# Performance work log

Hardware: AMD Instinct MI355X
Metric: run time of the kernel (lower is better)

The kernel has to match this reference:

```python
import jax, jax.numpy as jnp
import numpy as np

TOP_K = 2


def setup_inputs() -> dict:
    key = jax.random.key(0)
    ks = jax.random.split(key, 5)
    B, S, D, F, E = 4, 2048, 1024, 2048, 8
    sd = 1.0 / np.sqrt(D)
    sf = 1.0 / np.sqrt(F)
    return {
        "hidden_states": jax.random.normal(ks[0], (B, S, D), jnp.float32),
        "router_w1": jax.random.normal(ks[1], (D, 128), jnp.float32) * sd,
        "router_w2": jax.random.normal(ks[2], (128, E), jnp.float32) * (1.0 / np.sqrt(128)),
        "W1": jax.random.normal(ks[3], (E, D, F), jnp.float32) * sd,
        "W2": jax.random.normal(ks[4], (E, F, D), jnp.float32) * sf,
    }


def reference(hidden_states, router_w1, router_w2, W1, W2):
    B, S, D = hidden_states.shape
    E = W1.shape[0]
    # --- Router: MLP -> softmax -> top-k -> renormalize ---
    router_logits = jax.nn.silu(hidden_states @ router_w1) @ router_w2  # (B,S,E)
    router_probs = jax.nn.softmax(router_logits, axis=-1)
    top_vals, top_idx = jax.lax.top_k(router_probs, TOP_K)  # (B,S,K)
    routing_weights = top_vals / jnp.sum(top_vals, axis=-1, keepdims=True)

    # --- Dispatch/combine as dense combine-weight matrix (faithful to
    # weighted scatter-add combine in _grouped_expert_forward) ---
    T = B * S
    x = hidden_states.reshape(T, D)
    idx = top_idx.reshape(T, TOP_K)
    w = routing_weights.reshape(T, TOP_K).astype(hidden_states.dtype)
    combine = jnp.zeros((T, E), hidden_states.dtype).at[
        jnp.arange(T)[:, None], idx
    ].add(w)  # (T,E)

    # --- Per-expert FFN on all tokens, then weighted combine ---
    h = jax.nn.silu(jnp.einsum("td,edf->tef", x, W1))  # (T,E,F)
    expert_out = jnp.einsum("tef,efd->ted", h, W2)      # (T,E,D)
    out = jnp.einsum("te,ted->td", combine, expert_out)
    return out.reshape(B, S, D)
```

## Files before the change

### kernel.cpp

```cpp
#include <hip/hip_runtime.h>
#include <hip/hip_bf16.h>
#include <math.h>

#define T_TOK 8192
#define E_NUM 8
#define GAP_TAU 2e-3f

typedef __attribute__((ext_vector_type(8))) short short8;
typedef __attribute__((ext_vector_type(4))) float floatx4;

__device__ __forceinline__ unsigned short f2bf(float f) {
  unsigned int u = __builtin_bit_cast(unsigned int, f);
  u += 0x7fffu + ((u >> 16) & 1u);
  return (unsigned short)(u >> 16);
}

__device__ __forceinline__ void async16(const unsigned short* g, unsigned short* l) {
  __builtin_amdgcn_global_load_lds(
      (const __attribute__((address_space(1))) void*)g,
      (__attribute__((address_space(3))) void*)l, 16, 0, 0);
}

__device__ __forceinline__ bool tile_map(int flat, const int* cnt, int nt_log2,
                                         int& e, int& m0, int& n0) {
  const int xcd = flat & 7;
  const int idx = flat >> 3;
  int mtp[E_NUM + 1];
  mtp[0] = 0;
#pragma unroll
  for (int q = 0; q < E_NUM; ++q) mtp[q + 1] = mtp[q] + ((cnt[q] + 127) >> 7);
  const int MT = mtp[E_NUM];
  const int band = (MT + 7) >> 3;
  const int i = idx >> nt_log2;
  if (i >= band) return false;
  const int g = xcd * band + i;
  if (g >= MT) return false;
  e = 0;
#pragma unroll
  for (int q = 0; q < E_NUM - 1; ++q) if (g >= mtp[q + 1]) e = q + 1;
  m0 = (g - mtp[e]) << 7;
  n0 = (idx & ((1 << nt_log2) - 1)) << 7;
  return true;
}

__global__ __launch_bounds__(256) void router_fp32_kernel(
    const float* __restrict__ x, const float* __restrict__ rw1,
    const float* __restrict__ rw2,
    int* __restrict__ tok_top, float* __restrict__ tok_w,
    int* __restrict__ fix_list, int* __restrict__ fix_cnt,
    unsigned short* __restrict__ xb) {
  __shared__ __align__(16) float xs[8][1024];
  __shared__ float ph[128][8];
  __shared__ float hs[8][129];
  __shared__ float ls[8][8];
  const int t = threadIdx.x;
  const int tok0 = blockIdx.x * 8;

  {
    const float4* xsrc = (const float4*)(x + (size_t)tok0 * 1024);
    float4* xd = (float4*)&xs[0][0];
    ushort4* xbd = (ushort4*)(xb + (size_t)tok0 * 1024);
#pragma unroll
    for (int i = 0; i < 8; ++i) {
      float4 v = xsrc[t + i * 256];
      xd[t + i * 256] = v;
      ushort4 o;
      o.x = f2bf(v.x); o.y = f2bf(v.y); o.z = f2bf(v.z); o.w = f2bf(v.w);
      xbd[t + i * 256] = o;
    }
  }
  __syncthreads();

  const int j = t & 127, h = t >> 7;
  float acc[8];
#pragma unroll
  for (int tt = 0; tt < 8; ++tt) acc[tt] = 0.f;

  const int dbeg = h * 512, dend = dbeg + 512;
#pragma unroll 2
  for (int d0 = dbeg; d0 < dend; d0 += 4) {
    float w0 = rw1[(d0 + 0) * 128 + j];
    float w1 = rw1[(d0 + 1) * 128 + j];
    float w2 = rw1[(d0 + 2) * 128 + j];
    float w3 = rw1[(d0 + 3) * 128 + j];
    float4 xv[8];
#pragma unroll
    for (int tt = 0; tt < 8; ++tt) xv[tt] = *(const float4*)&xs[tt][d0];
#pragma unroll
    for (int tt = 0; tt < 8; ++tt) {
      acc[tt] = fmaf(xv[tt].x, w0, acc[tt]);
      acc[tt] = fmaf(xv[tt].y, w1, acc[tt]);
      acc[tt] = fmaf(xv[tt].z, w2, acc[tt]);
      acc[tt] = fmaf(xv[tt].w, w3, acc[tt]);
    }
  }
  if (h == 1) {
#pragma unroll
    for (int tt = 0; tt < 8; ++tt) ph[j][tt] = acc[tt];
  }
  __syncthreads();
  if (h == 0) {
#pragma unroll
    for (int tt = 0; tt < 8; ++tt) {
      float a = acc[tt] + ph[j][tt];
      hs[tt][j] = a / (1.f + expf(-a));
    }
  }
  __syncthreads();
  if (t < 64) {
    int tt = t >> 3, e = t & 7;
    float l = 0.f;
#pragma unroll 4
    for (int jj = 0; jj < 128; ++jj) l = fmaf(hs[tt][jj], rw2[jj * 8 + e], l);
    ls[tt][e] = l;
  }
  __syncthreads();
  if (t < 8) {
    int tt = t;
    float l[8];
#pragma unroll
    for (int e = 0; e < 8; ++e) l[e] = ls[tt][e];
    int i0 = 0;
#pragma unroll
    for (int e = 1; e < 8; ++e) if (l[e] > l[i0]) i0 = e;
    int i1 = (i0 == 0) ? 1 : 0;
#pragma unroll
    for (int e = 0; e < 8; ++e) if (e != i0 && l[e] > l[i1]) i1 = e;
    float v2 = -3.4e38f;
#pragma unroll
    for (int e = 0; e < 8; ++e) if (e != i0 && e != i1 && l[e] > v2) v2 = l[e];
    float gap = l[i1] - v2;
    float p = expf(l[i1] - l[i0]);
    float w0 = 1.f / (1.f + p);
    int tok = tok0 + tt;
    tok_top[2 * tok] = i0; tok_top[2 * tok + 1] = i1;
    tok_w[2 * tok] = w0;   tok_w[2 * tok + 1] = 1.f - w0;
    if (gap < GAP_TAU) { int pos = atomicAdd(fix_cnt, 1); fix_list[pos] = tok; }
  }
}

__global__ __launch_bounds__(256) void router_fix_kernel(
    const float* __restrict__ x, const float* __restrict__ rw1,
    const float* __restrict__ rw2, const int* __restrict__ fix_list,
    const int* __restrict__ fix_cnt,
    int* __restrict__ tok_top, float* __restrict__ tok_w) {
  __shared__ __align__(16) float xs[1024];
  __shared__ double red[128];
  __shared__ double hs[128];
  __shared__ double ls[8];
  const int t = threadIdx.x;
  const int nfix = *fix_cnt;
  for (int it = blockIdx.x; it < nfix; it += gridDim.x) {
    int tok = fix_list[it];
    ((float4*)xs)[t] = ((const float4*)(x + (size_t)tok * 1024))[t];
    __syncthreads();
    const int j = t & 127, h = t >> 7;
    double a0 = 0, a1 = 0, a2 = 0, a3 = 0;
    const int dbeg = h * 512;
    for (int d0 = dbeg; d0 < dbeg + 512; d0 += 4) {
      a0 = fma((double)xs[d0 + 0], (double)rw1[(d0 + 0) * 128 + j], a0);
      a1 = fma((double)xs[d0 + 1], (double)rw1[(d0 + 1) * 128 + j], a1);
      a2 = fma((double)xs[d0 + 2], (double)rw1[(d0 + 2) * 128 + j], a2);
      a3 = fma((double)xs[d0 + 3], (double)rw1[(d0 + 3) * 128 + j], a3);
    }
    double a = (a0 + a1) + (a2 + a3);
    if (h == 1) red[j] = a;
    __syncthreads();
    if (h == 0) {
      double s = a + red[j];
      hs[j] = s / (1.0 + exp(-s));
    }
    __syncthreads();
    if (t < 8) {
      int e = t;
      double l = 0;
      for (int jj = 0; jj < 128; ++jj) l = fma(hs[jj], (double)rw2[jj * 8 + e], l);
      ls[e] = l;
    }
    __syncthreads();
    if (t == 0) {
      double l[8];
#pragma unroll
      for (int e = 0; e < 8; ++e) l[e] = ls[e];
      int i0 = 0;
#pragma unroll
      for (int e = 1; e < 8; ++e) if (l[e] > l[i0]) i0 = e;
      int i1 = (i0 == 0) ? 1 : 0;
#pragma unroll
      for (int e = 0; e < 8; ++e) if (e != i0 && l[e] > l[i1]) i1 = e;
      double p = exp(l[i1] - l[i0]);
      double w0 = 1.0 / (1.0 + p);
      tok_top[2 * tok] = i0; tok_top[2 * tok + 1] = i1;
      tok_w[2 * tok] = (float)w0; tok_w[2 * tok + 1] = (float)(1.0 - w0);
    }
    __syncthreads();
  }
}

__global__ __launch_bounds__(256) void scatter_kernel(
    const int* __restrict__ tok_top, const float* __restrict__ tok_w,
    int* __restrict__ cnt, int* __restrict__ tid_list, float* __restrict__ tw_list) {
  __shared__ int hist[8], run[8];
  const int t = threadIdx.x;
  if (t < 8) hist[t] = 0;
  __syncthreads();
  const int tok = blockIdx.x * 256 + t;
  const int e0 = tok_top[2 * tok], e1 = tok_top[2 * tok + 1];
  atomicAdd(&hist[e0], 1);
  atomicAdd(&hist[e1], 1);
  __syncthreads();
  if (t < 8) run[t] = atomicAdd(&cnt[t], hist[t]);
  __syncthreads();
  int p0 = atomicAdd(&run[e0], 1);
  tid_list[e0 * T_TOK + p0] = tok; tw_list[e0 * T_TOK + p0] = tok_w[2 * tok];
  int p1 = atomicAdd(&run[e1], 1);
  tid_list[e1 * T_TOK + p1] = tok; tw_list[e1 * T_TOK + p1] = tok_w[2 * tok + 1];
}

__global__ void prefix_kernel(const int* __restrict__ cnt, int* __restrict__ base) {
  if (threadIdx.x == 0 && blockIdx.x == 0) {
    int s = 0;
    for (int e = 0; e < E_NUM; ++e) { base[e] = s; s += cnt[e]; }
  }
}

__global__ __launch_bounds__(256) void transpose_bf16_kernel(
    const float* __restrict__ in, unsigned short* __restrict__ out, int R, int C) {
  __shared__ unsigned short tile[64][65];
  const int e = blockIdx.z;
  const int r0 = blockIdx.y * 64, c0 = blockIdx.x * 64;
  const float* src = in + (size_t)e * R * C;
  unsigned short* dst = out + (size_t)e * R * C;
  const int t = threadIdx.x;
  const int cc = (t & 15) * 4;
#pragma unroll
  for (int p = 0; p < 4; ++p) {
    int r = p * 16 + (t >> 4);
    float4 v = *(const float4*)(src + (size_t)(r0 + r) * C + c0 + cc);
    tile[cc + 0][r] = f2bf(v.x);
    tile[cc + 1][r] = f2bf(v.y);
    tile[cc + 2][r] = f2bf(v.z);
    tile[cc + 3][r] = f2bf(v.w);
  }
  __syncthreads();
#pragma unroll
  for (int p = 0; p < 4; ++p) {
    int fr = p * 16 + (t >> 4);
    ushort4 o;
    o.x = tile[fr][cc + 0]; o.y = tile[fr][cc + 1];
    o.z = tile[fr][cc + 2]; o.w = tile[fr][cc + 3];
    *(ushort4*)(dst + (size_t)(c0 + fr) * R + r0 + cc) = o;
  }
}

__global__ __launch_bounds__(256) void gemm1_kernel(
    const unsigned short* __restrict__ xb,
    const unsigned short* __restrict__ w1t,
    const int* __restrict__ cnt, const int* __restrict__ base,
    const int* __restrict__ tid_list,
    unsigned short* __restrict__ h_buf) {
  int e, m0, n0;
  if (!tile_map(blockIdx.x, cnt, 4, e, m0, n0)) return;
  const int count = cnt[e];
  const int bs = base[e];

  __shared__ __align__(16) unsigned short As[128 * 64];
  __shared__ __align__(16) unsigned short Bs[128 * 64];

  const int t = threadIdx.x;
  const int wv = t >> 6, lane = t & 63;
  const int quad = lane >> 4, lr = lane & 15;
  const int wm = (wv & 1) * 64, wn = (wv >> 1) * 64;
  const int lr8 = lane >> 3, lc8 = lane & 7;
  const int chunk = lc8 ^ lr8;

  const unsigned short* aptr[4];
  const unsigned short* bptr[4];
#pragma unroll
  for (int q = 0; q < 4; ++q) {
    int ar = m0 + wv * 32 + q * 8 + lr8;
    int ai = ar < count ? ar : count - 1;
    int tok = tid_list[e * T_TOK + ai];
    aptr[q] = xb + (size_t)tok * 1024 + chunk * 8;
    int br = n0 + wv * 32 + q * 8 + lr8;
    bptr[q] = w1t + ((size_t)e * 2048 + br) * 1024 + chunk * 8;
  }
  unsigned short* aldsb = &As[wv * 2048];
  unsigned short* bldsb = &Bs[wv * 2048];

  floatx4 zero = {0.f, 0.f, 0.f, 0.f};
  floatx4 acc[4][4];
#pragma unroll
  for (int i = 0; i < 4; ++i)
#pragma unroll
    for (int j = 0; j < 4; ++j) acc[i][j] = zero;

  for (int k0 = 0; k0 < 1024; k0 += 64) {
    __syncthreads();
#pragma unroll
    for (int q = 0; q < 4; ++q) {
      async16(aptr[q] + k0, aldsb + q * 512);
      async16(bptr[q] + k0, bldsb + q * 512);
    }
    __syncthreads();
#pragma unroll
    for (int ks = 0; ks < 2; ++ks) {
      short8 af[4], bfv[4];
#pragma unroll
      for (int i = 0; i < 4; ++i) {
        int r = wm + i * 16 + lr;
        int pc = (ks * 4 + quad) ^ (lr & 7);
        af[i] = *(const short8*)&As[r * 64 + pc * 8];
      }
#pragma unroll
      for (int j = 0; j < 4; ++j) {
        int r = wn + j * 16 + lr;
        int pc = (ks * 4 + quad) ^ (lr & 7);
        bfv[j] = *(const short8*)&Bs[r * 64 + pc * 8];
      }
#pragma unroll
      for (int i = 0; i < 4; ++i)
#pragma unroll
        for (int j = 0; j < 4; ++j)
          acc[i][j] = __builtin_amdgcn_mfma_f32_16x16x32_bf16(af[i], bfv[j], acc[i][j], 0, 0, 0);
    }
  }

#pragma unroll
  for (int i = 0; i < 4; ++i) {
#pragma unroll
    for (int r = 0; r < 4; ++r) {
      int grow = m0 + wm + i * 16 + quad * 4 + r;
      if (grow < count) {
        size_t rowoff = (size_t)(bs + grow) * 2048;
#pragma unroll
        for (int j = 0; j < 4; ++j) {
          float v = acc[i][j][r];
          float s = v / (1.0f + __expf(-v));
          h_buf[rowoff + n0 + wn + j * 16 + lr] = f2bf(s);
        }
      }
    }
  }
}

__global__ __launch_bounds__(256) void gemm2_kernel(
    const unsigned short* __restrict__ h_buf,
    const unsigned short* __restrict__ w2t,
    const int* __restrict__ cnt, const int* __restrict__ base,
    const int* __restrict__ tid_list, const float* __restrict__ tw_list,
    float* __restrict__ out) {
  int e, m0, n0;
  if (!tile_map(blockIdx.x, cnt, 3, e, m0, n0)) return;
  const int count = cnt[e];
  const int bs = base[e];

  __shared__ __align__(16) unsigned short As[128 * 64];
  __shared__ __align__(16) unsigned short Bs[128 * 64];

  const int t = threadIdx.x;
  const int wv = t >> 6, lane = t & 63;
  const int quad = lane >> 4, lr = lane & 15;
  const int wm = (wv & 1) * 64, wn = (wv >> 1) * 64;
  const int lr8 = lane >> 3, lc8 = lane & 7;
  const int chunk = lc8 ^ lr8;

  const unsigned short* aptr[4];
  const unsigned short* bptr[4];
#pragma unroll
  for (int q = 0; q < 4; ++q) {
    int ar = m0 + wv * 32 + q * 8 + lr8;
    int ai = ar < count ? ar : count - 1;
    aptr[q] = h_buf + (size_t)(bs + ai) * 2048 + chunk * 8;
    int br = n0 + wv * 32 + q * 8 + lr8;
    bptr[q] = w2t + ((size_t)e * 1024 + br) * 2048 + chunk * 8;
  }
  unsigned short* aldsb = &As[wv * 2048];
  unsigned short* bldsb = &Bs[wv * 2048];

  floatx4 zero = {0.f, 0.f, 0.f, 0.f};
  floatx4 acc[4][4];
#pragma unroll
  for (int i = 0; i < 4; ++i)
#pragma unroll
    for (int j = 0; j < 4; ++j) acc[i][j] = zero;

  for (int k0 = 0; k0 < 2048; k0 += 64) {
    __syncthreads();
#pragma unroll
    for (int q = 0; q < 4; ++q) {
      async16(aptr[q] + k0, aldsb + q * 512);
      async16(bptr[q] + k0, bldsb + q * 512);
    }
    __syncthreads();
#pragma unroll
    for (int ks = 0; ks < 2; ++ks) {
      short8 af[4], bfv[4];
#pragma unroll
      for (int i = 0; i < 4; ++i) {
        int r = wm + i * 16 + lr;
        int pc = (ks * 4 + quad) ^ (lr & 7);
        af[i] = *(const short8*)&As[r * 64 + pc * 8];
      }
#pragma unroll
      for (int j = 0; j < 4; ++j) {
        int r = wn + j * 16 + lr;
        int pc = (ks * 4 + quad) ^ (lr & 7);
        bfv[j] = *(const short8*)&Bs[r * 64 + pc * 8];
      }
#pragma unroll
      for (int i = 0; i < 4; ++i)
#pragma unroll
        for (int j = 0; j < 4; ++j)
          acc[i][j] = __builtin_amdgcn_mfma_f32_16x16x32_bf16(af[i], bfv[j], acc[i][j], 0, 0, 0);
    }
  }

#pragma unroll
  for (int i = 0; i < 4; ++i) {
#pragma unroll
    for (int r = 0; r < 4; ++r) {
      int grow = m0 + wm + i * 16 + quad * 4 + r;
      if (grow < count) {
        int tok = tid_list[e * T_TOK + grow];
        float w = tw_list[e * T_TOK + grow];
        size_t rowoff = (size_t)tok * 1024;
#pragma unroll
        for (int j = 0; j < 4; ++j) {
          unsafeAtomicAdd(&out[rowoff + n0 + wn + j * 16 + lr], acc[i][j][r] * w);
        }
      }
    }
  }
}

extern "C" void kernel_launch(void* const* d_in, const int* in_sizes, int n_in,
                              void* d_out, int out_size, void* d_ws, size_t ws_size,
                              hipStream_t stream) {
  const float* x   = (const float*)d_in[0];
  const float* rw1 = (const float*)d_in[1];
  const float* rw2 = (const float*)d_in[2];
  const float* W1  = (const float*)d_in[3];
  const float* W2  = (const float*)d_in[4];
  float* out = (float*)d_out;

  char* ws = (char*)d_ws;
  int*            cnt      = (int*)(ws + 0);
  int*            base     = (int*)(ws + 64);
  int*            fix_cnt  = (int*)(ws + 128);
  int*            tid_list = (int*)(ws + 512);
  float*          tw_list  = (float*)(ws + 262656);
  unsigned short* xb       = (unsigned short*)(ws + 524800);
  unsigned short* w1t      = (unsigned short*)(ws + 17302016);
  unsigned short* w2t      = (unsigned short*)(ws + 50856448);
  unsigned short* hbuf     = (unsigned short*)(ws + 84410880);
  int*            tok_top  = (int*)(ws + 151519744);
  float*          tok_w    = (float*)(ws + 151585280);
  int*            fix_list = (int*)(ws + 151650816);

  hipMemsetAsync(d_out, 0, (size_t)T_TOK * 1024 * 4, stream);
  hipMemsetAsync(ws, 0, 192, stream);

  hipLaunchKernelGGL(router_fp32_kernel, dim3(1024), dim3(256), 0, stream,
                     x, rw1, rw2, tok_top, tok_w, fix_list, fix_cnt, xb);
  hipLaunchKernelGGL(router_fix_kernel, dim3(128), dim3(256), 0, stream,
                     x, rw1, rw2, fix_list, fix_cnt, tok_top, tok_w);
  hipLaunchKernelGGL(scatter_kernel, dim3(32), dim3(256), 0, stream,
                     tok_top, tok_w, cnt, tid_list, tw_list);
  hipLaunchKernelGGL(prefix_kernel, dim3(1), dim3(1), 0, stream, cnt, base);
  hipLaunchKernelGGL(transpose_bf16_kernel, dim3(32, 16, 8), dim3(256), 0, stream,
                     W1, w1t, 1024, 2048);
  hipLaunchKernelGGL(transpose_bf16_kernel, dim3(16, 32, 8), dim3(256), 0, stream,
                     W2, w2t, 2048, 1024);
  hipLaunchKernelGGL(gemm1_kernel, dim3(2176), dim3(256), 0, stream,
                     xb, w1t, cnt, base, tid_list, hbuf);
  hipLaunchKernelGGL(gemm2_kernel, dim3(1088), dim3(256), 0, stream,
                     hbuf, w2t, cnt, base, tid_list, tw_list, out);
}
```

Before: 552.5 us.

## Prefetch next K tile into registers in expert GEMMs, drop prefix kernel

Both grouped GEMM kernels replace direct global-to-LDS async loads with register-staged loads. The next K tile is loaded into registers while MFMAs run on the current LDS tile, then written to swizzled LDS between barriers. This is meant to hide global memory latency behind compute. Separately, the per-expert base offsets are now computed inside tile_map from the counts, which removes the single-thread prefix kernel launch. The trade-off is more VGPR pressure from holding the prefetch buffers and the extra LDS store instructions.

Result: slower. 1.019 ms (+84.4%).

```diff
diff --git a/kernel.cpp b/kernel.cpp
--- a/kernel.cpp
+++ b/kernel.cpp
@@ -15,20 +15,18 @@
   return (unsigned short)(u >> 16);
 }
 
-__device__ __forceinline__ void async16(const unsigned short* g, unsigned short* l) {
-  __builtin_amdgcn_global_load_lds(
-      (const __attribute__((address_space(1))) void*)g,
-      (__attribute__((address_space(3))) void*)l, 16, 0, 0);
-}
-
 __device__ __forceinline__ bool tile_map(int flat, const int* cnt, int nt_log2,
-                                         int& e, int& m0, int& n0) {
+                                         int& e, int& m0, int& n0, int& bs) {
   const int xcd = flat & 7;
   const int idx = flat >> 3;
-  int mtp[E_NUM + 1];
-  mtp[0] = 0;
-#pragma unroll
-  for (int q = 0; q < E_NUM; ++q) mtp[q + 1] = mtp[q] + ((cnt[q] + 127) >> 7);
+  int c[E_NUM], mtp[E_NUM + 1], tkp[E_NUM + 1];
+  mtp[0] = 0; tkp[0] = 0;
+#pragma unroll
+  for (int q = 0; q < E_NUM; ++q) {
+    c[q] = cnt[q];
+    mtp[q + 1] = mtp[q] + ((c[q] + 127) >> 7);
+    tkp[q + 1] = tkp[q] + c[q];
+  }
   const int MT = mtp[E_NUM];
   const int band = (MT + 7) >> 3;
   const int i = idx >> nt_log2;
@@ -40,6 +38,7 @@
   for (int q = 0; q < E_NUM - 1; ++q) if (g >= mtp[q + 1]) e = q + 1;
   m0 = (g - mtp[e]) << 7;
   n0 = (idx & ((1 << nt_log2) - 1)) << 7;
+  bs = tkp[e];
   return true;
 }
 
@@ -217,13 +216,6 @@
   tid_list[e1 * T_TOK + p1] = tok; tw_list[e1 * T_TOK + p1] = tok_w[2 * tok + 1];
 }
 
-__global__ void prefix_kernel(const int* __restrict__ cnt, int* __restrict__ base) {
-  if (threadIdx.x == 0 && blockIdx.x == 0) {
-    int s = 0;
-    for (int e = 0; e < E_NUM; ++e) { base[e] = s; s += cnt[e]; }
-  }
-}
-
 __global__ __launch_bounds__(256) void transpose_bf16_kernel(
     const float* __restrict__ in, unsigned short* __restrict__ out, int R, int C) {
   __shared__ unsigned short tile[64][65];
@@ -256,37 +248,37 @@
 __global__ __launch_bounds__(256) void gemm1_kernel(
     const unsigned short* __restrict__ xb,
     const unsigned short* __restrict__ w1t,
-    const int* __restrict__ cnt, const int* __restrict__ base,
-    const int* __restrict__ tid_list,
+    const int* __restrict__ cnt, const int* __restrict__ tid_list,
     unsigned short* __restrict__ h_buf) {
-  int e, m0, n0;
-  if (!tile_map(blockIdx.x, cnt, 4, e, m0, n0)) return;
+  int e, m0, n0, bs;
+  if (!tile_map(blockIdx.x, cnt, 4, e, m0, n0, bs)) return;
   const int count = cnt[e];
-  const int bs = base[e];
 
   __shared__ __align__(16) unsigned short As[128 * 64];
   __shared__ __align__(16) unsigned short Bs[128 * 64];
 
   const int t = threadIdx.x;
-  const int wv = t >> 6, lane = t & 63;
+  const int lane = t & 63;
+  const int wv = t >> 6;
   const int quad = lane >> 4, lr = lane & 15;
   const int wm = (wv & 1) * 64, wn = (wv >> 1) * 64;
-  const int lr8 = lane >> 3, lc8 = lane & 7;
-  const int chunk = lc8 ^ lr8;
-
-  const unsigned short* aptr[4];
-  const unsigned short* bptr[4];
+
+  const int row_l = t >> 3;
+  const int ck = t & 7;
+  const unsigned short* ag[4];
+  const unsigned short* bg[4];
+  int ldsw[4];
 #pragma unroll
   for (int q = 0; q < 4; ++q) {
-    int ar = m0 + wv * 32 + q * 8 + lr8;
+    int row = q * 32 + row_l;
+    int ar = m0 + row;
     int ai = ar < count ? ar : count - 1;
     int tok = tid_list[e * T_TOK + ai];
-    aptr[q] = xb + (size_t)tok * 1024 + chunk * 8;
-    int br = n0 + wv * 32 + q * 8 + lr8;
-    bptr[q] = w1t + ((size_t)e * 2048 + br) * 1024 + chunk * 8;
-  }
-  unsigned short* aldsb = &As[wv * 2048];
-  unsigned short* bldsb = &Bs[wv * 2048];
+    ag[q] = xb + (size_t)tok * 1024 + ck * 8;
+    int br = n0 + row;
+    bg[q] = w1t + ((size_t)e * 2048 + br) * 1024 + ck * 8;
+    ldsw[q] = row * 64 + ((ck ^ (row_l & 7)) * 8);
+  }
 
   floatx4 zero = {0.f, 0.f, 0.f, 0.f};
   floatx4 acc[4][4];
@@ -295,22 +287,34 @@
 #pragma unroll
     for (int j = 0; j < 4; ++j) acc[i][j] = zero;
 
-  for (int k0 = 0; k0 < 1024; k0 += 64) {
-    __syncthreads();
-#pragma unroll
-    for (int q = 0; q < 4; ++q) {
-      async16(aptr[q] + k0, aldsb + q * 512);
-      async16(bptr[q] + k0, bldsb + q * 512);
-    }
-    __syncthreads();
+  uint4 pa[4], pb[4];
+#pragma unroll
+  for (int q = 0; q < 4; ++q) { pa[q] = *(const uint4*)ag[q]; pb[q] = *(const uint4*)bg[q]; }
+#pragma unroll
+  for (int q = 0; q < 4; ++q) {
+    *(uint4*)&As[ldsw[q]] = pa[q];
+    *(uint4*)&Bs[ldsw[q]] = pb[q];
+  }
+  __syncthreads();
+
+  const int K = 1024;
+  for (int k0 = 0; k0 < K; k0 += 64) {
+    const bool more = (k0 + 64) < K;
+    if (more) {
+#pragma unroll
+      for (int q = 0; q < 4; ++q) {
+        pa[q] = *(const uint4*)(ag[q] + k0 + 64);
+        pb[q] = *(const uint4*)(bg[q] + k0 + 64);
+      }
+    }
 #pragma unroll
     for (int ks = 0; ks < 2; ++ks) {
       short8 af[4], bfv[4];
 #pragma unroll
-      for (int i = 0; i < 4; ++i) {
-        int r = wm + i * 16 + lr;
+      for (int ii = 0; ii < 4; ++ii) {
+        int r = wm + ii * 16 + lr;
         int pc = (ks * 4 + quad) ^ (lr & 7);
-        af[i] = *(const short8*)&As[r * 64 + pc * 8];
+        af[ii] = *(const short8*)&As[r * 64 + pc * 8];
       }
 #pragma unroll
       for (int j = 0; j < 4; ++j) {
@@ -319,10 +323,19 @@
         bfv[j] = *(const short8*)&Bs[r * 64 + pc * 8];
       }
 #pragma unroll
-      for (int i = 0; i < 4; ++i)
+      for (int ii = 0; ii < 4; ++ii)
 #pragma unroll
         for (int j = 0; j < 4; ++j)
-          acc[i][j] = __builtin_amdgcn_mfma_f32_16x16x32_bf16(af[i], bfv[j], acc[i][j], 0, 0, 0);
+          acc[ii][j] = __builtin_amdgcn_mfma_f32_16x16x32_bf16(af[ii], bfv[j], acc[ii][j], 0, 0, 0);
+    }
+    if (more) {
+      __syncthreads();
+#pragma unroll
+      for (int q = 0; q < 4; ++q) {
+        *(uint4*)&As[ldsw[q]] = pa[q];
+        *(uint4*)&Bs[ldsw[q]] = pb[q];
+      }
+      __syncthreads();
     }
   }
 
@@ -347,36 +360,37 @@
 __global__ __launch_bounds__(256) void gemm2_kernel(
     const unsigned short* __restrict__ h_buf,
     const unsigned short* __restrict__ w2t,
-    const int* __restrict__ cnt, const int* __restrict__ base,
-    const int* __restrict__ tid_list, const float* __restrict__ tw_list,
+    const int* __restrict__ cnt, const int* __restrict__ tid_list,
+    const float* __restrict__ tw_list,
     float* __restrict__ out) {
-  int e, m0, n0;
-  if (!tile_map(blockIdx.x, cnt, 3, e, m0, n0)) return;
+  int e, m0, n0, bs;
+  if (!tile_map(blockIdx.x, cnt, 3, e, m0, n0, bs)) return;
   const int count = cnt[e];
-  const int bs = base[e];
 
   __shared__ __align__(16) unsigned short As[128 * 64];
   __shared__ __align__(16) unsigned short Bs[128 * 64];
 
   const int t = threadIdx.x;
-  const int wv = t >> 6, lane = t & 63;
+  const int lane = t & 63;
+  const int wv = t >> 6;
   const int quad = lane >> 4, lr = lane & 15;
   const int wm = (wv & 1) * 64, wn = (wv >> 1) * 64;
-  const int lr8 = lane >> 3, lc8 = lane & 7;
-  const int chunk = lc8 ^ lr8;
-
-  const unsigned short* aptr[4];
-  const unsigned short* bptr[4];
+
+  const int row_l = t >> 3;
+  const int ck = t & 7;
+  const unsigned short* ag[4];
+  const unsigned short* bg[4];
+  int ldsw[4];
 #pragma unroll
   for (int q = 0; q < 4; ++q) {
-    int ar = m0 + wv * 32 + q * 8 + lr8;
+    int row = q * 32 + row_l;
+    int ar = m0 + row;
     int ai = ar < count ? ar : count - 1;
-    aptr[q] = h_buf + (size_t)(bs + ai) * 2048 + chunk * 8;
-    int br = n0 + wv * 32 + q * 8 + lr8;
-    bptr[q] = w2t + ((size_t)e * 1024 + br) * 2048 + chunk * 8;
-  }
-  unsigned short* aldsb = &As[wv * 2048];
-  unsigned short* bldsb = &Bs[wv * 2048];
+    ag[q] = h_buf + (size_t)(bs + ai) * 2048 + ck * 8;
+    int br = n0 + row;
+    bg[q] = w2t + ((size_t)e * 1024 + br) * 2048 + ck * 8;
+    ldsw[q] = row * 64 + ((ck ^ (row_l & 7)) * 8);
+  }
 
   floatx4 zero = {0.f, 0.f, 0.f, 0.f};
   floatx4 acc[4][4];
@@ -385,22 +399,34 @@
 #pragma unroll
     for (int j = 0; j < 4; ++j) acc[i][j] = zero;
 
-  for (int k0 = 0; k0 < 2048; k0 += 64) {
-    __syncthreads();
-#pragma unroll
-    for (int q = 0; q < 4; ++q) {
-      async16(aptr[q] + k0, aldsb + q * 512);
-      async16(bptr[q] + k0, bldsb + q * 512);
-    }
-    __syncthreads();
+  uint4 pa[4], pb[4];
+#pragma unroll
+  for (int q = 0; q < 4; ++q) { pa[q] = *(const uint4*)ag[q]; pb[q] = *(const uint4*)bg[q]; }
+#pragma unroll
+  for (int q = 0; q < 4; ++q) {
+    *(uint4*)&As[ldsw[q]] = pa[q];
+    *(uint4*)&Bs[ldsw[q]] = pb[q];
+  }
+  __syncthreads();
+
+  const int K = 2048;
+  for (int k0 = 0; k0 < K; k0 += 64) {
+    const bool more = (k0 + 64) < K;
+    if (more) {
+#pragma unroll
+      for (int q = 0; q < 4; ++q) {
+        pa[q] = *(const uint4*)(ag[q] + k0 + 64);
+        pb[q] = *(const uint4*)(bg[q] + k0 + 64);
+      }
+    }
 #pragma unroll
     for (int ks = 0; ks < 2; ++ks) {
       short8 af[4], bfv[4];
 #pragma unroll
-      for (int i = 0; i < 4; ++i) {
-        int r = wm + i * 16 + lr;
+      for (int ii = 0; ii < 4; ++ii) {
+        int r = wm + ii * 16 + lr;
         int pc = (ks * 4 + quad) ^ (lr & 7);
-        af[i] = *(const short8*)&As[r * 64 + pc * 8];
+        af[ii] = *(const short8*)&As[r * 64 + pc * 8];
       }
 #pragma unroll
       for (int j = 0; j < 4; ++j) {
@@ -409,10 +435,19 @@
         bfv[j] = *(const short8*)&Bs[r * 64 + pc * 8];
       }
 #pragma unroll
-      for (int i = 0; i < 4; ++i)
+      for (int ii = 0; ii < 4; ++ii)
 #pragma unroll
         for (int j = 0; j < 4; ++j)
-          acc[i][j] = __builtin_amdgcn_mfma_f32_16x16x32_bf16(af[i], bfv[j], acc[i][j], 0, 0, 0);
+          acc[ii][j] = __builtin_amdgcn_mfma_f32_16x16x32_bf16(af[ii], bfv[j], acc[ii][j], 0, 0, 0);
+    }
+    if (more) {
+      __syncthreads();
+#pragma unroll
+      for (int q = 0; q < 4; ++q) {
+        *(uint4*)&As[ldsw[q]] = pa[q];
+        *(uint4*)&Bs[ldsw[q]] = pb[q];
+      }
+      __syncthreads();
     }
   }
 
@@ -446,7 +481,6 @@
 
   char* ws = (char*)d_ws;
   int*            cnt      = (int*)(ws + 0);
-  int*            base     = (int*)(ws + 64);
   int*            fix_cnt  = (int*)(ws + 128);
   int*            tid_list = (int*)(ws + 512);
   float*          tw_list  = (float*)(ws + 262656);
@@ -467,13 +501,12 @@
                      x, rw1, rw2, fix_list, fix_cnt, tok_top, tok_w);
   hipLaunchKernelGGL(scatter_kernel, dim3(32), dim3(256), 0, stream,
                      tok_top, tok_w, cnt, tid_list, tw_list);
-  hipLaunchKernelGGL(prefix_kernel, dim3(1), dim3(1), 0, stream, cnt, base);
   hipLaunchKernelGGL(transpose_bf16_kernel, dim3(32, 16, 8), dim3(256), 0, stream,
                      W1, w1t, 1024, 2048);
   hipLaunchKernelGGL(transpose_bf16_kernel, dim3(16, 32, 8), dim3(256), 0, stream,
                      W2, w2t, 2048, 1024);
   hipLaunchKernelGGL(gemm1_kernel, dim3(2176), dim3(256), 0, stream,
-                     xb, w1t, cnt, base, tid_list, hbuf);
+                     xb, w1t, cnt, tid_list, hbuf);
   hipLaunchKernelGGL(gemm2_kernel, dim3(1088), dim3(256), 0, stream,
-                     hbuf, w2t, cnt, base, tid_list, tw_list, out);
-}
+                     hbuf, w2t, cnt, tid_list, tw_list, out);
+}
```
